# Performance work log

Hardware: AMD Instinct MI355X
Metric: run time of the kernel (lower is better)

Reference implementation:

```python
import jax, jax.numpy as jnp
import numpy as np

IMG = 224
PATCH = 16
EMBED = 768
C = 12
B = 64

def setup_inputs() -> dict:
    key = jax.random.key(0)
    k1, k2 = jax.random.split(key)
    x = jax.random.normal(k1, (B, C, IMG, IMG), dtype=jnp.float32)
    channel_weights = jax.random.normal(k2, (C, EMBED), dtype=jnp.float32)
    return {"x": x, "channel_weights": channel_weights}

def reference(x, channel_weights):
    # Original torch code builds a [E, C, K, K] conv weight by replicating each
    # channel_weights[c, e] across the full KxK kernel, then does a stride-K conv.
    # That is mathematically a per-patch KxK sum-pool followed by a C->E matmul.
    Bb, Cc, H, W = x.shape
    K = PATCH
    n = H // K  # patches per side (14)
    # [B, C, n, K, n, K] -> sum over kernel dims -> [B, C, n, n]
    pooled = x.reshape(Bb, Cc, n, K, n, K).sum(axis=(3, 5))
    # contract channel dim with [C, E] weights -> [B, n, n, E]
    out = jnp.einsum('bcij,ce->bije', pooled, channel_weights)
    return out.reshape(Bb, n * n, EMBED)
```

## Files before the change

kernel.cpp:

```cpp
#include <hip/hip_runtime.h>


#define BATCH 64
#define CH    12
#define IMGD  224
#define NP    14
#define NPP   (NP * NP)
#define EMB   768

__global__ __launch_bounds__(192) void dcsp_fused_kernel(
    const float* __restrict__ x,
    const float* __restrict__ w,
    float* __restrict__ out)
{
    const int blk = blockIdx.x;
    const int b = blk / NPP;
    const int p = blk - b * NPP;
    const int i = p / NP;
    const int j = p - i * NP;

    const int t    = threadIdx.x;
    const int lane = t & 63;
    const int wave = t >> 6;

    __shared__ float pooled[CH];

    const int r = lane >> 2;
    const int q = lane & 3;
    const int row = i * 16 + r;
    const int col = j * 16 + q * 4;

    float s[4];
#pragma unroll
    for (int k = 0; k < 4; ++k) {
        const int c = wave + 3 * k;
        const float4 v = *reinterpret_cast<const float4*>(
            x + (((size_t)(b * CH + c) * IMGD + row) * IMGD + col));
        s[k] = (v.x + v.y) + (v.z + v.w);
    }

#pragma unroll
    for (int off = 32; off > 0; off >>= 1) {
#pragma unroll
        for (int k = 0; k < 4; ++k)
            s[k] += __shfl_down(s[k], off, 64);
    }
    if (lane == 0) {
#pragma unroll
        for (int k = 0; k < 4; ++k)
            pooled[wave + 3 * k] = s[k];
    }
    __syncthreads();

    float4 acc = make_float4(0.f, 0.f, 0.f, 0.f);
    const float4* __restrict__ w4 = reinterpret_cast<const float4*>(w);
#pragma unroll
    for (int c = 0; c < CH; ++c) {
        const float  pc = pooled[c];
        const float4 wv = w4[c * (EMB / 4) + t];
        acc.x += pc * wv.x;
        acc.y += pc * wv.y;
        acc.z += pc * wv.z;
        acc.w += pc * wv.w;
    }
    reinterpret_cast<float4*>(out)[(size_t)blk * (EMB / 4) + t] = acc;
}

extern "C" void kernel_launch(void* const* d_in, const int* in_sizes, int n_in,
                              void* d_out, int out_size, void* d_ws, size_t ws_size,
                              hipStream_t stream) {
    const float* x = (const float*)d_in[0];
    const float* w = (const float*)d_in[1];
    float* out = (float*)d_out;

    dcsp_fused_kernel<<<BATCH * NPP, 192, 0, stream>>>(x, w, out);
}
```

Before: 229.6 us.

## Process two adjacent patches per block to widen loads and reuse weights

Each block now handles two horizontally adjacent patches with 384 threads. Every wave pools two channels across 128-byte row segments, and an xor-shuffle reduction keeps the two patch sums separate. The C->E weight reads are shared across two patches, halving weight traffic and the block count. The trade-off is larger blocks, a more complex lane-to-patch mapping, and less parallelism per block count.

```diff
diff --git a/kernel.cpp b/kernel.cpp
--- a/kernel.cpp
+++ b/kernel.cpp
@@ -7,63 +7,75 @@
 #define NP    14
 #define NPP   (NP * NP)
 #define EMB   768
+#define E4    (EMB / 4)
 
-__global__ __launch_bounds__(192) void dcsp_fused_kernel(
+__global__ __launch_bounds__(384) void dcsp_fused_kernel(
     const float* __restrict__ x,
     const float* __restrict__ w,
     float* __restrict__ out)
 {
     const int blk = blockIdx.x;
-    const int b = blk / NPP;
-    const int p = blk - b * NPP;
-    const int i = p / NP;
-    const int j = p - i * NP;
+    const int b  = blk / (NP * (NP / 2));
+    const int r0 = blk - b * (NP * (NP / 2));
+    const int i  = r0 / (NP / 2);
+    const int jj = r0 - i * (NP / 2);
 
     const int t    = threadIdx.x;
     const int lane = t & 63;
     const int wave = t >> 6;
 
-    __shared__ float pooled[CH];
+    __shared__ float pooled[2][CH];
 
-    const int r = lane >> 2;
-    const int q = lane & 3;
-    const int row = i * 16 + r;
-    const int col = j * 16 + q * 4;
+    const int r8 = lane >> 3;
+    const int q  = lane & 7;
+    const int colbase = jj * 32 + q * 4;
 
-    float s[4];
+    float s[2] = {0.f, 0.f};
 #pragma unroll
-    for (int k = 0; k < 4; ++k) {
-        const int c = wave + 3 * k;
-        const float4 v = *reinterpret_cast<const float4*>(
-            x + (((size_t)(b * CH + c) * IMGD + row) * IMGD + col));
-        s[k] = (v.x + v.y) + (v.z + v.w);
+    for (int k = 0; k < 2; ++k) {
+        const int c = wave * 2 + k;
+        const size_t chbase = (size_t)(b * CH + c) * IMGD * IMGD;
+#pragma unroll
+        for (int half = 0; half < 2; ++half) {
+            const int row = i * 16 + half * 8 + r8;
+            const float4 v = *reinterpret_cast<const float4*>(
+                x + chbase + (size_t)row * IMGD + colbase);
+            s[k] += (v.x + v.y) + (v.z + v.w);
+        }
     }
 
 #pragma unroll
-    for (int off = 32; off > 0; off >>= 1) {
+    for (int m = 0; m < 5; ++m) {
+        const int mask = (1 << m) < 4 ? (1 << m) : (1 << (m + 1));
 #pragma unroll
-        for (int k = 0; k < 4; ++k)
-            s[k] += __shfl_down(s[k], off, 64);
+        for (int k = 0; k < 2; ++k)
+            s[k] += __shfl_xor(s[k], mask, 64);
     }
     if (lane == 0) {
-#pragma unroll
-        for (int k = 0; k < 4; ++k)
-            pooled[wave + 3 * k] = s[k];
+        pooled[0][wave * 2 + 0] = s[0];
+        pooled[0][wave * 2 + 1] = s[1];
+    } else if (lane == 4) {
+        pooled[1][wave * 2 + 0] = s[0];
+        pooled[1][wave * 2 + 1] = s[1];
     }
     __syncthreads();
+
+    const int patch = t / E4;
+    const int e4    = t - patch * E4;
 
     float4 acc = make_float4(0.f, 0.f, 0.f, 0.f);
     const float4* __restrict__ w4 = reinterpret_cast<const float4*>(w);
 #pragma unroll
     for (int c = 0; c < CH; ++c) {
-        const float  pc = pooled[c];
-        const float4 wv = w4[c * (EMB / 4) + t];
+        const float  pc = pooled[patch][c];
+        const float4 wv = w4[c * E4 + e4];
         acc.x += pc * wv.x;
         acc.y += pc * wv.y;
         acc.z += pc * wv.z;
         acc.w += pc * wv.w;
     }
-    reinterpret_cast<float4*>(out)[(size_t)blk * (EMB / 4) + t] = acc;
+    const int j = jj * 2 + patch;
+    reinterpret_cast<float4*>(out)[((size_t)(b * NPP) + i * NP + j) * E4 + e4] = acc;
 }
 
 extern "C" void kernel_launch(void* const* d_in, const int* in_sizes, int n_in,
@@ -73,5 +85,5 @@
     const float* w = (const float*)d_in[1];
     float* out = (float*)d_out;
 
-    dcsp_fused_kernel<<<BATCH * NPP, 192, 0, stream>>>(x, w, out);
+    dcsp_fused_kernel<<<BATCH * NP * (NP / 2), 384, 0, stream>>>(x, w, out);
 }
```

After: 226.9 us. No clear change (-1.2%).

## Split fused pool+matmul into row-strip pooling kernel and persistent matmul kernel

Applied to the files above, without the earlier changes.

Replaces the single fused kernel (one block per patch doing pooling then a C->E matvec) with two kernels. A pooling kernel has each block read a contiguous 16-row strip of one channel with coalesced float4 loads and reduce it to 14 patch sums in shared memory, written to workspace. A grid-strided matmul kernel keeps the 12x768 weight slice in registers and reuses it across many patches. The aim is fully contiguous reads of x and no repeated weight reloads per patch, at the cost of a second launch and a workspace round trip.

```diff
diff --git a/kernel.cpp b/kernel.cpp
--- a/kernel.cpp
+++ b/kernel.cpp
@@ -7,63 +7,81 @@
 #define NP    14
 #define NPP   (NP * NP)
 #define EMB   768
+#define E4    (EMB / 4)
 
-__global__ __launch_bounds__(192) void dcsp_fused_kernel(
-    const float* __restrict__ x,
-    const float* __restrict__ w,
-    float* __restrict__ out)
+__global__ __launch_bounds__(256) void pool_kernel(
+    const float* __restrict__ x, float* __restrict__ pooled)
 {
-    const int blk = blockIdx.x;
-    const int b = blk / NPP;
-    const int p = blk - b * NPP;
-    const int i = p / NP;
-    const int j = p - i * NP;
+    const int bci = blockIdx.x;
+    const int t   = threadIdx.x;
 
-    const int t    = threadIdx.x;
-    const int lane = t & 63;
-    const int wave = t >> 6;
+    __shared__ float part[896];
+    __shared__ float p2[NP * 16];
 
-    __shared__ float pooled[CH];
+    const float4* __restrict__ x4 =
+        reinterpret_cast<const float4*>(x) + (size_t)bci * 896;
 
-    const int r = lane >> 2;
-    const int q = lane & 3;
-    const int row = i * 16 + r;
-    const int col = j * 16 + q * 4;
-
-    float s[4];
-#pragma unroll
-    for (int k = 0; k < 4; ++k) {
-        const int c = wave + 3 * k;
-        const float4 v = *reinterpret_cast<const float4*>(
-            x + (((size_t)(b * CH + c) * IMGD + row) * IMGD + col));
-        s[k] = (v.x + v.y) + (v.z + v.w);
-    }
-
-#pragma unroll
-    for (int off = 32; off > 0; off >>= 1) {
-#pragma unroll
-        for (int k = 0; k < 4; ++k)
-            s[k] += __shfl_down(s[k], off, 64);
-    }
-    if (lane == 0) {
-#pragma unroll
-        for (int k = 0; k < 4; ++k)
-            pooled[wave + 3 * k] = s[k];
+    {
+        float4 a = x4[t];
+        float4 b = x4[t + 256];
+        float4 c = x4[t + 512];
+        part[t]       = (a.x + a.y) + (a.z + a.w);
+        part[t + 256] = (b.x + b.y) + (b.z + b.w);
+        part[t + 512] = (c.x + c.y) + (c.z + c.w);
+        if (t < 128) {
+            float4 d = x4[t + 768];
+            part[t + 768] = (d.x + d.y) + (d.z + d.w);
+        }
     }
     __syncthreads();
 
-    float4 acc = make_float4(0.f, 0.f, 0.f, 0.f);
+    if (t < NP * 16) {
+        const int j = t >> 4, r = t & 15;
+        const int o = r * 56 + j * 4;
+        p2[t] = (part[o] + part[o + 1]) + (part[o + 2] + part[o + 3]);
+    }
+    __syncthreads();
+
+    if (t < NP) {
+        float s = 0.f;
+#pragma unroll
+        for (int r = 0; r < 16; ++r) s += p2[t * 16 + r];
+        pooled[(size_t)bci * NP + t] = s;
+    }
+}
+
+__global__ __launch_bounds__(192) void mm_kernel(
+    const float* __restrict__ pooled, const float* __restrict__ w,
+    float* __restrict__ out)
+{
+    const int t = threadIdx.x;
     const float4* __restrict__ w4 = reinterpret_cast<const float4*>(w);
+
+    float4 wc[CH];
 #pragma unroll
-    for (int c = 0; c < CH; ++c) {
-        const float  pc = pooled[c];
-        const float4 wv = w4[c * (EMB / 4) + t];
-        acc.x += pc * wv.x;
-        acc.y += pc * wv.y;
-        acc.z += pc * wv.z;
-        acc.w += pc * wv.w;
+    for (int c = 0; c < CH; ++c) wc[c] = w4[c * E4 + t];
+
+    float4* __restrict__ o4 = reinterpret_cast<float4*>(out);
+
+    for (int bp = blockIdx.x; bp < BATCH * NPP; bp += gridDim.x) {
+        const int b = bp / NPP;
+        const int p = bp - b * NPP;
+        const float* __restrict__ pv = pooled + (size_t)b * (CH * NPP) + p;
+
+        float pc[CH];
+#pragma unroll
+        for (int c = 0; c < CH; ++c) pc[c] = pv[c * NPP];
+
+        float4 acc = make_float4(0.f, 0.f, 0.f, 0.f);
+#pragma unroll
+        for (int c = 0; c < CH; ++c) {
+            acc.x += pc[c] * wc[c].x;
+            acc.y += pc[c] * wc[c].y;
+            acc.z += pc[c] * wc[c].z;
+            acc.w += pc[c] * wc[c].w;
+        }
+        o4[(size_t)bp * E4 + t] = acc;
     }
-    reinterpret_cast<float4*>(out)[(size_t)blk * (EMB / 4) + t] = acc;
 }
 
 extern "C" void kernel_launch(void* const* d_in, const int* in_sizes, int n_in,
@@ -71,7 +89,9 @@
                               hipStream_t stream) {
     const float* x = (const float*)d_in[0];
     const float* w = (const float*)d_in[1];
-    float* out = (float*)d_out;
+    float* out    = (float*)d_out;
+    float* pooled = (float*)d_ws;
 
-    dcsp_fused_kernel<<<BATCH * NPP, 192, 0, stream>>>(x, w, out);
+    pool_kernel<<<BATCH * CH * NP, 256, 0, stream>>>(x, pooled);
+    mm_kernel<<<896, 192, 0, stream>>>(pooled, w, out);
 }
```

Measured after the change: 231.7 us. Within noise of the previous version (+0.9%).
